# Kernel tuning notes

Hardware: AMD Instinct MI355X
Metric: run time of the kernel (lower is better)

Reference implementation:

```python
import jax, jax.numpy as jnp
import numpy as np

N, C, E = 50000, 128, 10
INV3 = float(1.0 / np.sqrt(3.0))
NORM_C = float(1.0 / np.sqrt(C))


def setup_inputs() -> dict:
    key = jax.random.key(0)
    ks = jax.random.split(key, 14)
    node_feats = jax.random.normal(ks[0], (N, 4 * C), jnp.float32)
    elem = jax.random.randint(ks[1], (N,), 0, E)
    node_attrs = jax.nn.one_hot(elem, E, dtype=jnp.float32)
    sc = jax.random.normal(ks[2], (N, 4 * C), jnp.float32)
    tp2_w = jax.random.normal(ks[3], (4, C), jnp.float32)
    tp3_w = jax.random.normal(ks[4], (8, C), jnp.float32)
    coef0_w0 = jax.random.normal(ks[5], (E, C, C), jnp.float32)
    coef0_w1 = jax.random.normal(ks[6], (E, C, C), jnp.float32)
    coef1_w0 = jax.random.normal(ks[7], (E, 2 * C, C), jnp.float32)
    coef1_w1 = jax.random.normal(ks[8], (E, 2 * C, C), jnp.float32)
    coef2_w0 = jax.random.normal(ks[9], (E, 4 * C, C), jnp.float32)
    coef2_w1 = jax.random.normal(ks[10], (E, 4 * C, C), jnp.float32)
    lin_w0 = jax.random.normal(ks[11], (C, C), jnp.float32)
    lin_w1 = jax.random.normal(ks[12], (C, C), jnp.float32)
    return dict(node_feats=node_feats, node_attrs=node_attrs, sc=sc,
                tp2_w=tp2_w, tp3_w=tp3_w,
                coef0_w0=coef0_w0, coef0_w1=coef0_w1,
                coef1_w0=coef1_w0, coef1_w1=coef1_w1,
                coef2_w0=coef2_w0, coef2_w1=coef2_w1,
                lin_w0=lin_w0, lin_w1=lin_w1)


def acc_elem_linear(x0, x1, attrs, W0, W1):
    # per-element linear combine: one-hot attrs select element-specific weights
    norm = 1.0 / np.sqrt(x0.shape[1])
    o0 = jnp.zeros((attrs.shape[0], W0.shape[2]), x0.dtype)
    o1 = jnp.zeros((attrs.shape[0], W1.shape[2], 3), x1.dtype)
    for e in range(W0.shape[0]):  # small fixed element count
        a = attrs[:, e]
        o0 = o0 + a[:, None] * (x0 @ W0[e])
        o1 = o1 + a[:, None, None] * jnp.einsum('ncm,cd->ndm', x1, W1[e])
    return o0 * norm, o1 * norm


def reference(node_feats, node_attrs, sc, tp2_w, tp3_w,
              coef0_w0, coef0_w1, coef1_w0, coef1_w1,
              coef2_w0, coef2_w1, lin_w0, lin_w1):
    n = node_feats.shape[0]
    s = node_feats[:, :C]                      # [N,C]    0e
    v = node_feats[:, C:].reshape(n, C, 3)     # [N,C,3]  1o

    # nu=2: channelwise (uuu) CG tensor product, paths filtered to {0e,1o}
    m0a = tp2_w[0] * s * s                                # 0e x 0e -> 0e
    m1a = tp2_w[1][:, None] * s[:, :, None] * v * INV3    # 0e x 1o -> 1o
    m1b = tp2_w[2][:, None] * v * s[:, :, None] * INV3    # 1o x 0e -> 1o
    m0b = tp2_w[3] * jnp.sum(v * v, axis=-1) * INV3       # 1o x 1o -> 0e

    # nu=3: mid (A0=m0a 0e, A1=m1a 1o, A2=m1b 1o, A3=m0b 0e) x node_feats
    q0 = jnp.concatenate([
        tp3_w[0] * m0a * s,
        tp3_w[3] * jnp.sum(m1a * v, -1) * INV3,
        tp3_w[5] * jnp.sum(m1b * v, -1) * INV3,
        tp3_w[6] * m0b * s], axis=1)                      # [N,4C]
    q1 = jnp.concatenate([
        tp3_w[1][:, None] * m0a[:, :, None] * v * INV3,
        tp3_w[2][:, None] * m1a * s[:, :, None] * INV3,
        tp3_w[4][:, None] * m1b * s[:, :, None] * INV3,
        tp3_w[7][:, None] * m0b[:, :, None] * v * INV3], axis=1)  # [N,4C,3]

    f0, f1 = acc_elem_linear(s, v, node_attrs, coef0_w0, coef0_w1)
    g0, g1 = acc_elem_linear(jnp.concatenate([m0a, m0b], 1),
                             jnp.concatenate([m1a, m1b], 1),
                             node_attrs, coef1_w0, coef1_w1)
    h0, h1 = acc_elem_linear(q0, q1, node_attrs, coef2_w0, coef2_w1)
    o0 = f0 + g0 + h0
    o1 = f1 + g1 + h1

    o0 = (o0 @ lin_w0) * NORM_C
    o1 = jnp.einsum('ncm,cd->ndm', o1, lin_w1) * NORM_C
    out = jnp.concatenate([o0, o1.reshape(n, -1)], axis=1) + sc
    return out
```

## Files before the change

### kernel.cpp

```cpp
#include <hip/hip_runtime.h>

typedef unsigned short u16;
typedef __attribute__((ext_vector_type(8))) short short8;
typedef __attribute__((ext_vector_type(4))) float f32x4;

#define N_NODES 50000
#define C_ 128
#define E_ 10
#define NT_ 16
#define NBLK_MAIN 3200
#define K0_ 640
#define K1_ 512

#define WF0_BYTES (E_ * 8 * 20 * 512 * 2)
#define WF1_BYTES (E_ * 8 * 16 * 512 * 2)
#define CNT_OFF   (WF0_BYTES + WF1_BYTES)
#define STARTS_OFF (CNT_OFF + 64)
#define LIST_OFF  (STARTS_OFF + 64)

__device__ __forceinline__ u16 f2bf(float f){ union{unsigned u; float f;} v; v.f = f; unsigned u = v.u; u += 0x7FFFu + ((u>>16)&1u); return (u16)(u>>16); }

__global__ void zero_cnt_kernel(int* __restrict__ cnt) {
    if (threadIdx.x < E_) cnt[threadIdx.x] = 0;
}

__global__ void prep_weights_kernel(
    const float* __restrict__ tp2, const float* __restrict__ tp3,
    const float* __restrict__ c00, const float* __restrict__ c10, const float* __restrict__ c20,
    const float* __restrict__ c01, const float* __restrict__ c11, const float* __restrict__ c21,
    const float* __restrict__ lin0, const float* __restrict__ lin1,
    u16* __restrict__ WF0, u16* __restrict__ WF1)
{
    const int b = blockIdx.x;
    const int e = b / (K0_ + K1_);
    const int r = b % (K0_ + K1_);
    const int which = (r >= K0_) ? 1 : 0;
    const int k = which ? (r - K0_) : r;
    const int seg = k >> 7;
    const int c = k & 127;
    const int tid = threadIdx.x;

    const float i128 = 0.08838834764831845f;
    const float i256 = 0.0625f;
    const float i512 = 0.04419417382415922f;
    const float I3   = 0.5773502691896258f;
    const float I9   = I3 * I3;

    const float t2_0 = tp2[0*C_+c], t2_1 = tp2[1*C_+c], t2_2 = tp2[2*C_+c], t2_3 = tp2[3*C_+c];
    const float t3_0 = tp3[0*C_+c], t3_1 = tp3[1*C_+c], t3_2 = tp3[2*C_+c];
    const float t3_3 = tp3[3*C_+c], t3_4 = tp3[4*C_+c], t3_5 = tp3[5*C_+c];
    const float t3_6 = tp3[6*C_+c], t3_7 = tp3[7*C_+c];

    __shared__ float row[C_];
    const int jj = tid;
    float val;
    if (!which) {
        const float* C0 = c00 + e * C_   * C_;
        const float* C1 = c10 + e * 2*C_ * C_;
        const float* C2 = c20 + e * 4*C_ * C_;
        switch (seg) {
        case 0: val = i128 * C0[c*C_ + jj]; break;
        case 1: val = t2_0 * i256 * C1[c*C_ + jj]; break;
        case 2: val = t2_3 * I3 * i256 * C1[(C_+c)*C_ + jj]; break;
        case 3: val = t3_0 * t2_0 * i512 * C2[c*C_ + jj]; break;
        default: val = i512 * ( t3_3*t2_1*I9 * C2[(C_  +c)*C_ + jj]
                              + t3_5*t2_2*I9 * C2[(2*C_+c)*C_ + jj]
                              + t3_6*t2_3*I3 * C2[(3*C_+c)*C_ + jj] ); break;
        }
    } else {
        const float* C0 = c01 + e * C_   * C_;
        const float* C1 = c11 + e * 2*C_ * C_;
        const float* C2 = c21 + e * 4*C_ * C_;
        switch (seg) {
        case 0: val = i128 * C0[c*C_ + jj]; break;
        case 1: val = I3 * i256 * ( t2_1 * C1[c*C_ + jj]
                                  + t2_2 * C1[(C_+c)*C_ + jj] ); break;
        case 2: val = i512 * ( t3_1*t2_0*I3 * C2[c*C_ + jj]
                             + t3_2*t2_1*I9 * C2[(C_  +c)*C_ + jj]
                             + t3_4*t2_2*I9 * C2[(2*C_+c)*C_ + jj] ); break;
        default: val = i512 * t3_7*t2_3*I9 * C2[(3*C_+c)*C_ + jj]; break;
        }
    }
    row[jj] = val;
    __syncthreads();

    const float* lin = which ? lin1 : lin0;
    float acc = 0.f;
#pragma unroll 8
    for (int x = 0; x < C_; ++x) acc += row[x] * lin[x*C_ + tid];
    const float NC = 0.08838834764831845f;
    const u16 wv = f2bf(acc * NC);

    const int col = tid;
    const int w_ = col >> 4, lcol = col & 15;
    const int ks = (c >> 5), r2 = c & 31;
    const int eh = r2 >> 4, g = (r2 >> 2) & 3, el = r2 & 3;
    const int elem = eh*4 + el;
    const int lane = lcol + 16*g;
    if (!which) {
        const int slot = seg*4 + ks;
        WF0[(((size_t)(e*8 + w_))*20 + slot)*512 + lane*8 + elem] = wv;
    } else {
        const int slot = seg*4 + ks;
        WF1[(((size_t)(e*8 + w_))*16 + slot)*512 + lane*8 + elem] = wv;
    }
}

__global__ void bucket_kernel(const float* __restrict__ attrs,
                              int* __restrict__ cnt, int* __restrict__ lists)
{
    __shared__ int lcnt[E_];
    __shared__ int lbase[E_];
    const int n = blockIdx.x * 256 + threadIdx.x;
    if (threadIdx.x < E_) lcnt[threadIdx.x] = 0;
    __syncthreads();
    int e = 0, my = 0;
    if (n < N_NODES) {
        const float* a = attrs + (size_t)n * E_;
#pragma unroll
        for (int i = 0; i < E_; ++i) if (a[i] > 0.5f) e = i;
        my = atomicAdd(&lcnt[e], 1);
    }
    __syncthreads();
    if (threadIdx.x < E_) lbase[threadIdx.x] = atomicAdd(&cnt[threadIdx.x], lcnt[threadIdx.x]);
    __syncthreads();
    if (n < N_NODES) lists[e*N_NODES + lbase[e] + my] = n;
}

__global__ void plan_kernel(const int* __restrict__ cnt, int* __restrict__ starts) {
    if (threadIdx.x == 0) {
        int acc = 0;
        for (int e = 0; e < E_; ++e) { starts[e] = acc; acc += (cnt[e] + NT_ - 1) / NT_; }
        starts[E_] = acc;
    }
}

__global__ __launch_bounds__(512, 4) void main_kernel(
    const float* __restrict__ feats, const float* __restrict__ sc,
    const int* __restrict__ cnt, const int* __restrict__ starts,
    const int* __restrict__ lists,
    const u16* __restrict__ WF0, const u16* __restrict__ WF1,
    float* __restrict__ out)
{
    __shared__ __align__(16) u16 Afull[68 * 512];
    __shared__ int nodes_s[NT_];
    __shared__ int hdr[2];

    const int tid = threadIdx.x;
    const int bx = blockIdx.x;
    if (tid == 0) {
        if (bx >= starts[E_]) { hdr[0] = -1; hdr[1] = 0; }
        else {
            int e = 0;
            while (e < E_ - 1 && bx >= starts[e+1]) ++e;
            hdr[0] = e; hdr[1] = bx - starts[e];
        }
    }
    __syncthreads();
    const int e = hdr[0];
    if (e < 0) return;
    const int tile = hdr[1];
    const int nvalid = min(NT_, cnt[e] - tile * NT_);

    if (tid < NT_) nodes_s[tid] = (tid < nvalid) ? lists[e*N_NODES + tile*NT_ + tid] : -1;
    __syncthreads();

    {
        const int node = tid >> 5;
        const int cg   = tid & 31;
        const int n = nodes_s[node];
        float4 sv  = make_float4(0.f,0.f,0.f,0.f);
        float4 va  = sv, vb = sv, vc = sv;
        if (n >= 0) {
            const float* f = feats + (size_t)n * 512;
            sv = *(const float4*)(f + cg*4);
            va = *(const float4*)(f + 128 + cg*12);
            vb = *(const float4*)(f + 128 + cg*12 + 4);
            vc = *(const float4*)(f + 128 + cg*12 + 8);
        }
        float Sa[4]  = {sv.x, sv.y, sv.z, sv.w};
        float Va[12] = {va.x,va.y,va.z,va.w, vb.x,vb.y,vb.z,vb.w, vc.x,vc.y,vc.z,vc.w};

        u16 fsS[5][4];
        u16 fsV[4][3][4];
#pragma unroll
        for (int i = 0; i < 4; ++i) {
            const float S  = Sa[i];
            const float V0 = Va[3*i], V1 = Va[3*i+1], V2 = Va[3*i+2];
            const float S2 = S * S;
            const float VV = V0*V0 + V1*V1 + V2*V2;
            fsS[0][i] = f2bf(S);
            fsS[1][i] = f2bf(S2);
            fsS[2][i] = f2bf(VV);
            fsS[3][i] = f2bf(S2 * S);
            fsS[4][i] = f2bf(S * VV);
            const float Vm[3] = {V0, V1, V2};
#pragma unroll
            for (int m = 0; m < 3; ++m) {
                fsV[0][m][i] = f2bf(Vm[m]);
                fsV[1][m][i] = f2bf(S  * Vm[m]);
                fsV[2][m][i] = f2bf(S2 * Vm[m]);
                fsV[3][m][i] = f2bf(VV * Vm[m]);
            }
        }
        const int lane  = node + 16 * (cg & 3);
        const int ks    = cg >> 3;
        const int ebase = ((cg >> 2) & 1) * 4;
        const int lanep = lane ^ (ks << 1);
        u16* bp = &Afull[lanep*8 + ebase];
#pragma unroll
        for (int p = 0; p < 5; ++p)
            *(ushort4*)&bp[(p*4 + ks) * 512] = *(ushort4*)fsS[p];
#pragma unroll
        for (int q = 0; q < 4; ++q)
#pragma unroll
            for (int m = 0; m < 3; ++m)
                *(ushort4*)&bp[(20 + q*12 + m*4 + ks) * 512] = *(ushort4*)fsV[q][m];
    }
    __syncthreads();

    const int w = tid >> 6, l = tid & 63;
    const int lcol = l & 15, g = l >> 4;
    const int col = w*16 + lcol;
    const u16* WB0 = WF0 + ((size_t)(e*8 + w)) * 20 * 512;
    const u16* WB1 = WF1 + ((size_t)(e*8 + w)) * 16 * 512;

    f32x4 accS = {0.f, 0.f, 0.f, 0.f};
    f32x4 accV[3];
#pragma unroll
    for (int m = 0; m < 3; ++m) accV[m] = accS;

#pragma unroll
    for (int p = 0; p < 5; ++p) {
#pragma unroll
        for (int ks = 0; ks < 4; ++ks) {
            const int slot = p*4 + ks;
            const short8 b = *(const short8*)(WB0 + (size_t)slot*512 + l*8);
            const short8 a = *(const short8*)&Afull[(size_t)slot*512 + (l ^ (ks<<1))*8];
            accS = __builtin_amdgcn_mfma_f32_16x16x32_bf16(a, b, accS, 0, 0, 0);
        }
    }
#pragma unroll
    for (int q = 0; q < 4; ++q) {
#pragma unroll
        for (int ks = 0; ks < 4; ++ks) {
            const short8 b = *(const short8*)(WB1 + (size_t)(q*4 + ks)*512 + l*8);
            const int lp = (l ^ (ks<<1)) * 8;
#pragma unroll
            for (int m = 0; m < 3; ++m) {
                const short8 a = *(const short8*)&Afull[(size_t)(20 + q*12 + m*4 + ks)*512 + lp];
                accV[m] = __builtin_amdgcn_mfma_f32_16x16x32_bf16(a, b, accV[m], 0, 0, 0);
            }
        }
    }

    __syncthreads();
    float* OutB = (float*)Afull;
#pragma unroll
    for (int r = 0; r < 4; ++r) {
        const int node = 4*g + r;
        OutB[node*516 + col] = accS[r];
#pragma unroll
        for (int m = 0; m < 3; ++m)
            OutB[node*516 + 128 + 3*col + m] = accV[m][r];
    }
    __syncthreads();

    {
        const int node = tid >> 5;
        const int ch   = tid & 31;
        const int n = nodes_s[node];
        if (n >= 0) {
            const size_t gb = (size_t)n * 512;
#pragma unroll
            for (int j = 0; j < 4; ++j) {
                const int fo = ch*4 + 128*j;
                const float4 vres = *(const float4*)&OutB[node*516 + fo];
                const float4 s4   = *(const float4*)(sc + gb + fo);
                float4 o; o.x = vres.x + s4.x; o.y = vres.y + s4.y;
                o.z = vres.z + s4.z; o.w = vres.w + s4.w;
                *(float4*)(out + gb + fo) = o;
            }
        }
    }
}

extern "C" void kernel_launch(void* const* d_in, const int* in_sizes, int n_in,
                              void* d_out, int out_size, void* d_ws, size_t ws_size,
                              hipStream_t stream) {
    const float* feats = (const float*)d_in[0];
    const float* attrs = (const float*)d_in[1];
    const float* sc    = (const float*)d_in[2];
    const float* tp2   = (const float*)d_in[3];
    const float* tp3   = (const float*)d_in[4];
    const float* c00   = (const float*)d_in[5];
    const float* c01   = (const float*)d_in[6];
    const float* c10   = (const float*)d_in[7];
    const float* c11   = (const float*)d_in[8];
    const float* c20   = (const float*)d_in[9];
    const float* c21   = (const float*)d_in[10];
    const float* lin0  = (const float*)d_in[11];
    const float* lin1  = (const float*)d_in[12];
    float* out = (float*)d_out;

    char* ws = (char*)d_ws;
    u16* WF0   = (u16*)(ws);
    u16* WF1   = (u16*)(ws + WF0_BYTES);
    int* cnt   = (int*)(ws + CNT_OFF);
    int* starts= (int*)(ws + STARTS_OFF);
    int* lists = (int*)(ws + LIST_OFF);

    hipLaunchKernelGGL(zero_cnt_kernel, dim3(1), dim3(64), 0, stream, cnt);
    hipLaunchKernelGGL(prep_weights_kernel, dim3(E_*(K0_+K1_)), dim3(128), 0, stream,
                       tp2, tp3, c00, c10, c20, c01, c11, c21, lin0, lin1, WF0, WF1);
    hipLaunchKernelGGL(bucket_kernel, dim3((N_NODES + 255)/256), dim3(256), 0, stream,
                       attrs, cnt, lists);
    hipLaunchKernelGGL(plan_kernel, dim3(1), dim3(64), 0, stream, cnt, starts);
    hipLaunchKernelGGL(main_kernel, dim3(NBLK_MAIN), dim3(512), 0, stream,
                       feats, sc, cnt, starts, lists, WF0, WF1, out);
}
```

Measured before the change: 129.1 us.

## Use MFMA for weight prep, drop plan kernel, prefetch B fragments and skip

The weight-folding kernel is rewritten so each block builds a 128x128 bf16 tile of combined coefficients plus a transposed lin matrix in shared memory and multiplies them with MFMA, instead of one block per row doing scalar dot products. The plan kernel is removed and every main-kernel thread derives its element and tile from the counts directly. The main kernel double-buffers the B weight fragments across k-steps, loads the skip-connection values early, and drops two shared-memory syncs around node indices. Doing the lin product in bf16 instead of fp32 adds rounding error to the folded weights.

After: 118.2 us. 1.09x faster.

```diff
diff --git a/kernel.cpp b/kernel.cpp
--- a/kernel.cpp
+++ b/kernel.cpp
@@ -15,8 +15,7 @@
 #define WF0_BYTES (E_ * 8 * 20 * 512 * 2)
 #define WF1_BYTES (E_ * 8 * 16 * 512 * 2)
 #define CNT_OFF   (WF0_BYTES + WF1_BYTES)
-#define STARTS_OFF (CNT_OFF + 64)
-#define LIST_OFF  (STARTS_OFF + 64)
+#define LIST_OFF  (CNT_OFF + 64)
 
 __device__ __forceinline__ u16 f2bf(float f){ union{unsigned u; float f;} v; v.f = f; unsigned u = v.u; u += 0x7FFFu + ((u>>16)&1u); return (u16)(u>>16); }
 
@@ -24,7 +23,7 @@
     if (threadIdx.x < E_) cnt[threadIdx.x] = 0;
 }
 
-__global__ void prep_weights_kernel(
+__global__ __launch_bounds__(256) void prep_weights_kernel(
     const float* __restrict__ tp2, const float* __restrict__ tp3,
     const float* __restrict__ c00, const float* __restrict__ c10, const float* __restrict__ c20,
     const float* __restrict__ c01, const float* __restrict__ c11, const float* __restrict__ c21,
@@ -32,77 +31,135 @@
     u16* __restrict__ WF0, u16* __restrict__ WF1)
 {
     const int b = blockIdx.x;
-    const int e = b / (K0_ + K1_);
-    const int r = b % (K0_ + K1_);
-    const int which = (r >= K0_) ? 1 : 0;
-    const int k = which ? (r - K0_) : r;
-    const int seg = k >> 7;
-    const int c = k & 127;
+    const int e = b / 9, kb = b % 9;
+    const int which = (kb >= 5) ? 1 : 0;
+    const int seg = which ? kb - 5 : kb;
+    const float* __restrict__ lin = which ? lin1 : lin0;
+
+    __shared__ u16 R[128 * 136];
+    __shared__ u16 LT[128 * 132];
+
     const int tid = threadIdx.x;
-
-    const float i128 = 0.08838834764831845f;
-    const float i256 = 0.0625f;
-    const float i512 = 0.04419417382415922f;
-    const float I3   = 0.5773502691896258f;
-    const float I9   = I3 * I3;
-
-    const float t2_0 = tp2[0*C_+c], t2_1 = tp2[1*C_+c], t2_2 = tp2[2*C_+c], t2_3 = tp2[3*C_+c];
-    const float t3_0 = tp3[0*C_+c], t3_1 = tp3[1*C_+c], t3_2 = tp3[2*C_+c];
-    const float t3_3 = tp3[3*C_+c], t3_4 = tp3[4*C_+c], t3_5 = tp3[5*C_+c];
-    const float t3_6 = tp3[6*C_+c], t3_7 = tp3[7*C_+c];
-
-    __shared__ float row[C_];
-    const int jj = tid;
-    float val;
-    if (!which) {
-        const float* C0 = c00 + e * C_   * C_;
-        const float* C1 = c10 + e * 2*C_ * C_;
-        const float* C2 = c20 + e * 4*C_ * C_;
-        switch (seg) {
-        case 0: val = i128 * C0[c*C_ + jj]; break;
-        case 1: val = t2_0 * i256 * C1[c*C_ + jj]; break;
-        case 2: val = t2_3 * I3 * i256 * C1[(C_+c)*C_ + jj]; break;
-        case 3: val = t3_0 * t2_0 * i512 * C2[c*C_ + jj]; break;
-        default: val = i512 * ( t3_3*t2_1*I9 * C2[(C_  +c)*C_ + jj]
-                              + t3_5*t2_2*I9 * C2[(2*C_+c)*C_ + jj]
-                              + t3_6*t2_3*I3 * C2[(3*C_+c)*C_ + jj] ); break;
-        }
-    } else {
-        const float* C0 = c01 + e * C_   * C_;
-        const float* C1 = c11 + e * 2*C_ * C_;
-        const float* C2 = c21 + e * 4*C_ * C_;
-        switch (seg) {
-        case 0: val = i128 * C0[c*C_ + jj]; break;
-        case 1: val = I3 * i256 * ( t2_1 * C1[c*C_ + jj]
-                                  + t2_2 * C1[(C_+c)*C_ + jj] ); break;
-        case 2: val = i512 * ( t3_1*t2_0*I3 * C2[c*C_ + jj]
-                             + t3_2*t2_1*I9 * C2[(C_  +c)*C_ + jj]
-                             + t3_4*t2_2*I9 * C2[(2*C_+c)*C_ + jj] ); break;
-        default: val = i512 * t3_7*t2_3*I9 * C2[(3*C_+c)*C_ + jj]; break;
-        }
-    }
-    row[jj] = val;
-    __syncthreads();
-
-    const float* lin = which ? lin1 : lin0;
-    float acc = 0.f;
-#pragma unroll 8
-    for (int x = 0; x < C_; ++x) acc += row[x] * lin[x*C_ + tid];
     const float NC = 0.08838834764831845f;
-    const u16 wv = f2bf(acc * NC);
-
-    const int col = tid;
-    const int w_ = col >> 4, lcol = col & 15;
-    const int ks = (c >> 5), r2 = c & 31;
-    const int eh = r2 >> 4, g = (r2 >> 2) & 3, el = r2 & 3;
-    const int elem = eh*4 + el;
-    const int lane = lcol + 16*g;
-    if (!which) {
-        const int slot = seg*4 + ks;
-        WF0[(((size_t)(e*8 + w_))*20 + slot)*512 + lane*8 + elem] = wv;
-    } else {
-        const int slot = seg*4 + ks;
-        WF1[(((size_t)(e*8 + w_))*16 + slot)*512 + lane*8 + elem] = wv;
+
+    for (int t = tid; t < 128 * 32; t += 256) {
+        const int jj = t >> 5, c4 = (t & 31) << 2;
+        const float4 v = *(const float4*)(lin + jj * 128 + c4);
+        LT[(c4 + 0) * 132 + jj] = f2bf(v.x * NC);
+        LT[(c4 + 1) * 132 + jj] = f2bf(v.y * NC);
+        LT[(c4 + 2) * 132 + jj] = f2bf(v.z * NC);
+        LT[(c4 + 3) * 132 + jj] = f2bf(v.w * NC);
+    }
+
+    {
+        const int c = tid >> 1, jh = (tid & 1) * 64;
+        const float i128 = 0.08838834764831845f;
+        const float i256 = 0.0625f;
+        const float i512 = 0.04419417382415922f;
+        const float I3   = 0.5773502691896258f;
+        const float I9   = I3 * I3;
+        const float t2_0 = tp2[0*C_+c], t2_1 = tp2[1*C_+c], t2_2 = tp2[2*C_+c], t2_3 = tp2[3*C_+c];
+        const float t3_0 = tp3[0*C_+c], t3_1 = tp3[1*C_+c], t3_2 = tp3[2*C_+c];
+        const float t3_3 = tp3[3*C_+c], t3_4 = tp3[4*C_+c], t3_5 = tp3[5*C_+c];
+        const float t3_6 = tp3[6*C_+c], t3_7 = tp3[7*C_+c];
+
+        const float* P0; const float* P1 = nullptr; const float* P2 = nullptr;
+        float a0 = 0.f, a1 = 0.f, a2 = 0.f;
+        if (!which) {
+            const float* C0 = c00 + (size_t)e * C_   * C_;
+            const float* C1 = c10 + (size_t)e * 2*C_ * C_;
+            const float* C2 = c20 + (size_t)e * 4*C_ * C_;
+            switch (seg) {
+            case 0: P0 = C0 + c*C_;          a0 = i128; break;
+            case 1: P0 = C1 + c*C_;          a0 = t2_0 * i256; break;
+            case 2: P0 = C1 + (C_+c)*C_;     a0 = t2_3 * I3 * i256; break;
+            case 3: P0 = C2 + c*C_;          a0 = t3_0 * t2_0 * i512; break;
+            default:
+                P0 = C2 + (C_+c)*C_;         a0 = t3_3 * t2_1 * I9 * i512;
+                P1 = C2 + (2*C_+c)*C_;       a1 = t3_5 * t2_2 * I9 * i512;
+                P2 = C2 + (3*C_+c)*C_;       a2 = t3_6 * t2_3 * I3 * i512; break;
+            }
+        } else {
+            const float* C0 = c01 + (size_t)e * C_   * C_;
+            const float* C1 = c11 + (size_t)e * 2*C_ * C_;
+            const float* C2 = c21 + (size_t)e * 4*C_ * C_;
+            switch (seg) {
+            case 0: P0 = C0 + c*C_;          a0 = i128; break;
+            case 1: P0 = C1 + c*C_;          a0 = t2_1 * I3 * i256;
+                    P1 = C1 + (C_+c)*C_;     a1 = t2_2 * I3 * i256; break;
+            case 2: P0 = C2 + c*C_;          a0 = t3_1 * t2_0 * I3 * i512;
+                    P1 = C2 + (C_+c)*C_;     a1 = t3_2 * t2_1 * I9 * i512;
+                    P2 = C2 + (2*C_+c)*C_;   a2 = t3_4 * t2_2 * I9 * i512; break;
+            default: P0 = C2 + (3*C_+c)*C_;  a0 = t3_7 * t2_3 * I9 * i512; break;
+            }
+        }
+        for (int j4 = 0; j4 < 64; j4 += 4) {
+            const int jj = jh + j4;
+            const float4 v = *(const float4*)(P0 + jj);
+            float r0 = a0*v.x, r1 = a0*v.y, r2 = a0*v.z, r3 = a0*v.w;
+            if (P1) {
+                const float4 u = *(const float4*)(P1 + jj);
+                r0 += a1*u.x; r1 += a1*u.y; r2 += a1*u.z; r3 += a1*u.w;
+            }
+            if (P2) {
+                const float4 u = *(const float4*)(P2 + jj);
+                r0 += a2*u.x; r1 += a2*u.y; r2 += a2*u.z; r3 += a2*u.w;
+            }
+            ushort4 st; st.x = f2bf(r0); st.y = f2bf(r1); st.z = f2bf(r2); st.w = f2bf(r3);
+            *(ushort4*)&R[c * 136 + jj] = st;
+        }
+    }
+    __syncthreads();
+
+    const int wv = tid >> 6, l = tid & 63;
+    const int lcol = l & 15, gD = l >> 4;
+    f32x4 acc[2][8];
+#pragma unroll
+    for (int s = 0; s < 2; ++s)
+#pragma unroll
+        for (int t = 0; t < 8; ++t) acc[s][t] = (f32x4){0.f, 0.f, 0.f, 0.f};
+
+#pragma unroll
+    for (int ks2 = 0; ks2 < 4; ++ks2) {
+        const int jj0 = ks2 * 32 + gD * 4;
+        short8 bf[8];
+#pragma unroll
+        for (int t = 0; t < 8; ++t) {
+            const int colB = t * 16 + lcol;
+            union { unsigned long long q[2]; short8 v; } u;
+            u.q[0] = *(const unsigned long long*)&LT[colB * 132 + jj0];
+            u.q[1] = *(const unsigned long long*)&LT[colB * 132 + jj0 + 16];
+            bf[t] = u.v;
+        }
+#pragma unroll
+        for (int s = 0; s < 2; ++s) {
+            const int krow = (wv + s * 4) * 16 + lcol;
+            union { unsigned long long q[2]; short8 v; } ua;
+            ua.q[0] = *(const unsigned long long*)&R[krow * 136 + jj0];
+            ua.q[1] = *(const unsigned long long*)&R[krow * 136 + jj0 + 16];
+#pragma unroll
+            for (int t = 0; t < 8; ++t)
+                acc[s][t] = __builtin_amdgcn_mfma_f32_16x16x32_bf16(ua.v, bf[t], acc[s][t], 0, 0, 0);
+        }
+    }
+
+#pragma unroll
+    for (int s = 0; s < 2; ++s) {
+#pragma unroll
+        for (int r = 0; r < 4; ++r) {
+            const int k = (wv + s * 4) * 16 + 4 * gD + r;
+            const int ks = k >> 5, r2 = k & 31;
+            const int eh = r2 >> 4, g2 = (r2 >> 2) & 3, el = r2 & 3;
+            const int elem = eh * 4 + el;
+            const int lanef = lcol + 16 * g2;
+            const int slot = seg * 4 + ks;
+#pragma unroll
+            for (int t = 0; t < 8; ++t) {
+                const u16 wvl = f2bf(acc[s][t][r]);
+                if (!which) WF0[(((size_t)(e*8 + t))*20 + slot)*512 + lanef*8 + elem] = wvl;
+                else        WF1[(((size_t)(e*8 + t))*16 + slot)*512 + lanef*8 + elem] = wvl;
+            }
+        }
     }
 }
 
@@ -127,48 +184,34 @@
     if (n < N_NODES) lists[e*N_NODES + lbase[e] + my] = n;
 }
 
-__global__ void plan_kernel(const int* __restrict__ cnt, int* __restrict__ starts) {
-    if (threadIdx.x == 0) {
-        int acc = 0;
-        for (int e = 0; e < E_; ++e) { starts[e] = acc; acc += (cnt[e] + NT_ - 1) / NT_; }
-        starts[E_] = acc;
-    }
-}
-
 __global__ __launch_bounds__(512, 4) void main_kernel(
     const float* __restrict__ feats, const float* __restrict__ sc,
-    const int* __restrict__ cnt, const int* __restrict__ starts,
-    const int* __restrict__ lists,
+    const int* __restrict__ cnt, const int* __restrict__ lists,
     const u16* __restrict__ WF0, const u16* __restrict__ WF1,
     float* __restrict__ out)
 {
     __shared__ __align__(16) u16 Afull[68 * 512];
-    __shared__ int nodes_s[NT_];
-    __shared__ int hdr[2];
 
     const int tid = threadIdx.x;
     const int bx = blockIdx.x;
-    if (tid == 0) {
-        if (bx >= starts[E_]) { hdr[0] = -1; hdr[1] = 0; }
-        else {
-            int e = 0;
-            while (e < E_ - 1 && bx >= starts[e+1]) ++e;
-            hdr[0] = e; hdr[1] = bx - starts[e];
-        }
-    }
-    __syncthreads();
-    const int e = hdr[0];
+
+    int e = -1, tile = 0, accT = 0;
+#pragma unroll
+    for (int i = 0; i < E_; ++i) {
+        const int ci = cnt[i];
+        const int t = (ci + NT_ - 1) >> 4;
+        if (e < 0 && bx < accT + t) { e = i; tile = bx - accT; }
+        accT += t;
+    }
     if (e < 0) return;
-    const int tile = hdr[1];
     const int nvalid = min(NT_, cnt[e] - tile * NT_);
 
-    if (tid < NT_) nodes_s[tid] = (tid < nvalid) ? lists[e*N_NODES + tile*NT_ + tid] : -1;
-    __syncthreads();
+    const int node = tid >> 5;
+    const int ch   = tid & 31;
+    const int n = (node < nvalid) ? lists[e*N_NODES + tile*NT_ + node] : -1;
 
     {
-        const int node = tid >> 5;
-        const int cg   = tid & 31;
-        const int n = nodes_s[node];
+        const int cg = ch;
         float4 sv  = make_float4(0.f,0.f,0.f,0.f);
         float4 va  = sv, vb = sv, vc = sv;
         if (n >= 0) {
@@ -222,66 +265,80 @@
     const int w = tid >> 6, l = tid & 63;
     const int lcol = l & 15, g = l >> 4;
     const int col = w*16 + lcol;
-    const u16* WB0 = WF0 + ((size_t)(e*8 + w)) * 20 * 512;
-    const u16* WB1 = WF1 + ((size_t)(e*8 + w)) * 16 * 512;
+    const u16* WB0 = WF0 + ((size_t)(e*8 + w)) * 20 * 512 + l*8;
+    const u16* WB1 = WF1 + ((size_t)(e*8 + w)) * 16 * 512 + l*8;
 
     f32x4 accS = {0.f, 0.f, 0.f, 0.f};
     f32x4 accV[3];
 #pragma unroll
     for (int m = 0; m < 3; ++m) accV[m] = accS;
 
-#pragma unroll
-    for (int p = 0; p < 5; ++p) {
-#pragma unroll
-        for (int ks = 0; ks < 4; ++ks) {
-            const int slot = p*4 + ks;
-            const short8 b = *(const short8*)(WB0 + (size_t)slot*512 + l*8);
-            const short8 a = *(const short8*)&Afull[(size_t)slot*512 + (l ^ (ks<<1))*8];
-            accS = __builtin_amdgcn_mfma_f32_16x16x32_bf16(a, b, accS, 0, 0, 0);
-        }
-    }
-#pragma unroll
-    for (int q = 0; q < 4; ++q) {
-#pragma unroll
-        for (int ks = 0; ks < 4; ++ks) {
-            const short8 b = *(const short8*)(WB1 + (size_t)(q*4 + ks)*512 + l*8);
-            const int lp = (l ^ (ks<<1)) * 8;
+    float4 scR0, scR1, scR2, scR3;
+
+    short8 bS[2][5], bV[2][4];
+#pragma unroll
+    for (int p = 0; p < 5; ++p) bS[0][p] = *(const short8*)(WB0 + (p*4 + 0) * 512);
+#pragma unroll
+    for (int q = 0; q < 4; ++q) bV[0][q] = *(const short8*)(WB1 + (q*4 + 0) * 512);
+
+#pragma unroll
+    for (int ks = 0; ks < 4; ++ks) {
+        const int cur = ks & 1, nxt = cur ^ 1;
+        if (ks < 3) {
+#pragma unroll
+            for (int p = 0; p < 5; ++p) bS[nxt][p] = *(const short8*)(WB0 + (p*4 + ks + 1) * 512);
+#pragma unroll
+            for (int q = 0; q < 4; ++q) bV[nxt][q] = *(const short8*)(WB1 + (q*4 + ks + 1) * 512);
+        }
+        if (ks == 3 && n >= 0) {
+            const float* sp = sc + (size_t)n * 512 + ch * 4;
+            scR0 = *(const float4*)(sp);
+            scR1 = *(const float4*)(sp + 128);
+            scR2 = *(const float4*)(sp + 256);
+            scR3 = *(const float4*)(sp + 384);
+        }
+        const int lp8 = (l ^ (ks << 1)) * 8;
+#pragma unroll
+        for (int p = 0; p < 5; ++p) {
+            const short8 a = *(const short8*)&Afull[(p*4 + ks)*512 + lp8];
+            accS = __builtin_amdgcn_mfma_f32_16x16x32_bf16(a, bS[cur][p], accS, 0, 0, 0);
+        }
+#pragma unroll
+        for (int q = 0; q < 4; ++q)
 #pragma unroll
             for (int m = 0; m < 3; ++m) {
-                const short8 a = *(const short8*)&Afull[(size_t)(20 + q*12 + m*4 + ks)*512 + lp];
-                accV[m] = __builtin_amdgcn_mfma_f32_16x16x32_bf16(a, b, accV[m], 0, 0, 0);
-            }
-        }
+                const short8 a = *(const short8*)&Afull[(20 + q*12 + m*4 + ks)*512 + lp8];
+                accV[m] = __builtin_amdgcn_mfma_f32_16x16x32_bf16(a, bV[cur][q], accV[m], 0, 0, 0);
+            }
     }
 
     __syncthreads();
     float* OutB = (float*)Afull;
 #pragma unroll
     for (int r = 0; r < 4; ++r) {
-        const int node = 4*g + r;
-        OutB[node*516 + col] = accS[r];
+        const int nd = 4*g + r;
+        OutB[nd*516 + col] = accS[r];
 #pragma unroll
         for (int m = 0; m < 3; ++m)
-            OutB[node*516 + 128 + 3*col + m] = accV[m][r];
-    }
-    __syncthreads();
-
-    {
-        const int node = tid >> 5;
-        const int ch   = tid & 31;
-        const int n = nodes_s[node];
-        if (n >= 0) {
-            const size_t gb = (size_t)n * 512;
-#pragma unroll
-            for (int j = 0; j < 4; ++j) {
-                const int fo = ch*4 + 128*j;
-                const float4 vres = *(const float4*)&OutB[node*516 + fo];
-                const float4 s4   = *(const float4*)(sc + gb + fo);
-                float4 o; o.x = vres.x + s4.x; o.y = vres.y + s4.y;
-                o.z = vres.z + s4.z; o.w = vres.w + s4.w;
-                *(float4*)(out + gb + fo) = o;
-            }
-        }
+            OutB[nd*516 + 128 + 3*col + m] = accV[m][r];
+    }
+    __syncthreads();
+
+    if (n >= 0) {
+        const size_t gb = (size_t)n * 512 + ch * 4;
+        const float4 v0 = *(const float4*)&OutB[node*516 + ch*4];
+        const float4 v1 = *(const float4*)&OutB[node*516 + ch*4 + 128];
+        const float4 v2 = *(const float4*)&OutB[node*516 + ch*4 + 256];
+        const float4 v3 = *(const float4*)&OutB[node*516 + ch*4 + 384];
+        float4 o0, o1, o2, o3;
+        o0.x=v0.x+scR0.x; o0.y=v0.y+scR0.y; o0.z=v0.z+scR0.z; o0.w=v0.w+scR0.w;
+        o1.x=v1.x+scR1.x; o1.y=v1.y+scR1.y; o1.z=v1.z+scR1.z; o1.w=v1.w+scR1.w;
+        o2.x=v2.x+scR2.x; o2.y=v2.y+scR2.y; o2.z=v2.z+scR2.z; o2.w=v2.w+scR2.w;
+        o3.x=v3.x+scR3.x; o3.y=v3.y+scR3.y; o3.z=v3.z+scR3.z; o3.w=v3.w+scR3.w;
+        *(float4*)(out + gb)       = o0;
+        *(float4*)(out + gb + 128) = o1;
+        *(float4*)(out + gb + 256) = o2;
+        *(float4*)(out + gb + 384) = o3;
     }
 }
 
@@ -307,15 +364,13 @@
     u16* WF0   = (u16*)(ws);
     u16* WF1   = (u16*)(ws + WF0_BYTES);
     int* cnt   = (int*)(ws + CNT_OFF);
-    int* starts= (int*)(ws + STARTS_OFF);
     int* lists = (int*)(ws + LIST_OFF);
 
     hipLaunchKernelGGL(zero_cnt_kernel, dim3(1), dim3(64), 0, stream, cnt);
-    hipLaunchKernelGGL(prep_weights_kernel, dim3(E_*(K0_+K1_)), dim3(128), 0, stream,
+    hipLaunchKernelGGL(prep_weights_kernel, dim3(E_*9), dim3(256), 0, stream,
                        tp2, tp3, c00, c10, c20, c01, c11, c21, lin0, lin1, WF0, WF1);
     hipLaunchKernelGGL(bucket_kernel, dim3((N_NODES + 255)/256), dim3(256), 0, stream,
                        attrs, cnt, lists);
-    hipLaunchKernelGGL(plan_kernel, dim3(1), dim3(64), 0, stream, cnt, starts);
     hipLaunchKernelGGL(main_kernel, dim3(NBLK_MAIN), dim3(512), 0, stream,
-                       feats, sc, cnt, starts, lists, WF0, WF1, out);
-}
+                       feats, sc, cnt, lists, WF0, WF1, out);
+}
```
